# Kernel tuning notes

Measured on AMD Instinct MI355X. Metric: run time of the kernel, lower is better.

The kernel has to match this reference:

```python
import jax, jax.numpy as jnp
import numpy as np

N = 100000
E = 1600000
IN_FEATS = 512
N_HIDDEN = 128
N_CLASSES = 40


def setup_inputs() -> dict:
    key = jax.random.key(0)
    k1, k2, k3, k4, k5, k6, k7 = jax.random.split(key, 7)
    inputs = jax.random.normal(k1, (N, IN_FEATS), dtype=jnp.float32)
    edge_index = jax.random.randint(k2, (2, E), 0, N, dtype=jnp.int64)
    edge_attr = jax.random.uniform(k3, (E,), dtype=jnp.float32)
    # GCNConv params (Glorot-ish scaling)
    W1 = jax.random.normal(k4, (IN_FEATS, N_HIDDEN), dtype=jnp.float32) / np.sqrt(IN_FEATS)
    b1 = jnp.zeros((N_HIDDEN,), dtype=jnp.float32)
    W2 = jax.random.normal(k5, (N_HIDDEN, N_CLASSES), dtype=jnp.float32) / np.sqrt(N_HIDDEN)
    b2 = jnp.zeros((N_CLASSES,), dtype=jnp.float32)
    return {"inputs": inputs, "edge_index": edge_index, "edge_attr": edge_attr,
            "W1": W1, "b1": b1, "W2": W2, "b2": b2}


def gcn_conv(x, W, b, src, dst, edge_weight):
    """GCNConv with normalize=False: linear transform, then edge-weighted
    scatter-sum from src to dst, then bias."""
    m = x @ W                                   # [N, F_out]
    msgs = m[src] * edge_weight[:, None]        # gather + weight, [E, F_out]
    agg = jax.ops.segment_sum(msgs, dst, num_segments=x.shape[0])  # scatter-add
    return agg + b


def reference(inputs, edge_index, edge_attr, W1, b1, W2, b2):
    src, dst = edge_index[0], edge_index[1]
    h = jax.nn.relu(gcn_conv(inputs, W1, b1, src, dst, edge_attr))
    # F.dropout with training=False (eval mode) is identity -> deterministic baseline
    preds = gcn_conv(h, W2, b2, src, dst, edge_attr)
    return jax.nn.log_softmax(preds, axis=1)
```

## Files before the change

### kernel.cpp

```cpp
#include <hip/hip_runtime.h>
#include <hip/hip_bf16.h>
#include <cstdint>

#define N_NODES 100000
#define N_EDGES 1600000
#define F_IN    512
#define F_HID   128
#define F_OUT   40
#define F_OUT_PAD 48

#define BSH    8
#define NB     391
#define BEPT   8
#define BCHUNK 4096
#define GB     391
#define CONVB  140
#define FCAP   6144

typedef short v8s __attribute__((ext_vector_type(8)));
typedef float v4f __attribute__((ext_vector_type(4)));

__device__ __forceinline__ short f2bf(float f) {
    unsigned u = __float_as_uint(f);
    u += 0x7fffu + ((u >> 16) & 1u);
    return (short)(u >> 16);
}

__device__ __forceinline__ float bflo(unsigned u) { return __uint_as_float(u << 16); }
__device__ __forceinline__ float bfhi(unsigned u) { return __uint_as_float(u & 0xffff0000u); }

__device__ __forceinline__ v8s pack8(float4 a, float4 b) {
    v8s r;
    r[0] = f2bf(a.x); r[1] = f2bf(a.y); r[2] = f2bf(a.z); r[3] = f2bf(a.w);
    r[4] = f2bf(b.x); r[5] = f2bf(b.y); r[6] = f2bf(b.z); r[7] = f2bf(b.w);
    return r;
}

__device__ __forceinline__ void gload16(const void* g, void* l) {
    __builtin_amdgcn_global_load_lds(
        (const __attribute__((address_space(1))) void*)g,
        (__attribute__((address_space(3))) void*)l, 16, 0, 0);
}


__global__ __launch_bounds__(512) void k_bhist(const int* __restrict__ dst,
                                               int* __restrict__ bcnt,
                                               const float* __restrict__ W1,
                                               short* __restrict__ WT1,
                                               const float* __restrict__ W2,
                                               short* __restrict__ WT2) {
    if (blockIdx.x >= GB) {
        int i = (blockIdx.x - GB) * 512 + threadIdx.x;
        if (i < F_IN * F_HID) {
            int n = i >> 9, k = i & 511;
            WT1[i] = f2bf(W1[k * F_HID + n]);
        } else {
            int j = i - F_IN * F_HID;
            if (j < F_OUT_PAD * F_HID) {
                int n = j >> 7, k = j & 127;
                WT2[j] = (n < F_OUT) ? f2bf(W2[k * F_OUT + n]) : (short)0;
            }
        }
        return;
    }
    __shared__ int lh[512];
    int tid = threadIdx.x;
    lh[tid] = 0;
    __syncthreads();
    long e0 = (long)blockIdx.x * BCHUNK;
#pragma unroll
    for (int i = 0; i < BEPT; i++) {
        long e = e0 + tid + i * 512;
        if (e < N_EDGES) atomicAdd(&lh[dst[e] >> BSH], 1);
    }
    __syncthreads();
    if (tid < NB && lh[tid]) atomicAdd(&bcnt[tid], lh[tid]);
}

__global__ __launch_bounds__(512) void k_bscan(const int* __restrict__ bcnt,
                                               int* __restrict__ bbase,
                                               int* __restrict__ bcur) {
    __shared__ int sm[512];
    int tid = threadIdx.x;
    int v = (tid < NB) ? bcnt[tid] : 0;
    sm[tid] = v;
    __syncthreads();
    for (int off = 1; off < 512; off <<= 1) {
        int t = (tid >= off) ? sm[tid - off] : 0;
        __syncthreads();
        sm[tid] += t;
        __syncthreads();
    }
    if (tid < NB) {
        int ex = sm[tid] - v;
        bbase[tid] = ex;
        bcur[tid] = ex;
    }
    if (tid == 511) bbase[NB] = sm[511];
}

__global__ __launch_bounds__(512) void k_bscatter(const int* __restrict__ src,
                                                  const int* __restrict__ dst,
                                                  const float* __restrict__ w,
                                                  int* __restrict__ bcur,
                                                  int2* __restrict__ tmp) {
    __shared__ int cntA[512];
    __shared__ int ofsA[512];
    __shared__ int lcur[512];
    __shared__ int gb[512];
    __shared__ __align__(16) int2 recBuf[BCHUNK];
    __shared__ unsigned short bkt[BCHUNK];
    int tid = threadIdx.x;
    long e0 = (long)blockIdx.x * BCHUNK;
    cntA[tid] = 0;
    __syncthreads();

    int dloc[BEPT];
#pragma unroll
    for (int i = 0; i < BEPT; i++) {
        long e = e0 + tid + i * 512;
        int d = (e < N_EDGES) ? dst[e] : -1;
        dloc[i] = d;
        if (d >= 0) atomicAdd(&cntA[d >> BSH], 1);
    }
    __syncthreads();

    int v = cntA[tid];
    ofsA[tid] = v;
    __syncthreads();
    for (int off = 1; off < 512; off <<= 1) {
        int t = (tid >= off) ? ofsA[tid - off] : 0;
        __syncthreads();
        ofsA[tid] += t;
        __syncthreads();
    }
    int excl = ofsA[tid] - v;
    ofsA[tid] = excl;
    lcur[tid] = excl;
    if (tid < NB && v > 0) gb[tid] = atomicAdd(&bcur[tid], v);
    __syncthreads();

#pragma unroll
    for (int i = 0; i < BEPT; i++) {
        int d = dloc[i];
        if (d >= 0) {
            long e = e0 + tid + i * 512;
            int j = d >> BSH;
            int slot = atomicAdd(&lcur[j], 1);
            recBuf[slot] = make_int2(src[e] | ((d & 255) << 17), __float_as_int(w[e]));
            bkt[slot] = (unsigned short)j;
        }
    }
    __syncthreads();

    long rem = N_EDGES - e0;
    int total = (rem < BCHUNK) ? (int)rem : BCHUNK;
    for (int s = tid; s < total; s += 512) {
        int j = bkt[s];
        tmp[gb[j] + (s - ofsA[j])] = recBuf[s];
    }
}

__global__ __launch_bounds__(256) void k_fine(const int2* __restrict__ tmp,
                                              const int* __restrict__ bbase,
                                              int2* __restrict__ rec,
                                              int* __restrict__ rowptr,
                                              int* __restrict__ deg) {
    __shared__ int hist[256];
    __shared__ int ofs[256];
    __shared__ int cur[256];
    __shared__ __align__(16) int2 recOut[FCAP];
    int tid = threadIdx.x, b = blockIdx.x;
    int base = bbase[b];
    int cnt = bbase[b + 1] - base;

    hist[tid] = 0;
    __syncthreads();
    for (int i = tid; i < cnt; i += 256) {
        unsigned u = (unsigned)tmp[base + i].x;
        atomicAdd(&hist[u >> 17], 1);
    }
    __syncthreads();

    int v = hist[tid];
    ofs[tid] = v;
    __syncthreads();
    for (int off = 1; off < 256; off <<= 1) {
        int t = (tid >= off) ? ofs[tid - off] : 0;
        __syncthreads();
        ofs[tid] += t;
        __syncthreads();
    }
    int excl = ofs[tid] - v;
    ofs[tid] = excl;
    cur[tid] = excl;
    int node = (b << BSH) + tid;
    if (node < N_NODES) {
        rowptr[node] = base + excl;
        deg[node] = v;
    }
    __syncthreads();

    if (cnt <= FCAP) {
        for (int i = tid; i < cnt; i += 256) {
            int2 r = tmp[base + i];
            unsigned u = (unsigned)r.x;
            int slot = atomicAdd(&cur[u >> 17], 1);
            recOut[slot] = make_int2((int)(u & 0x1FFFFu), r.y);
        }
        __syncthreads();
        for (int i = tid; i < cnt; i += 256) rec[base + i] = recOut[i];
    } else {
        for (int i = tid; i < cnt; i += 256) {
            int2 r = tmp[base + i];
            unsigned u = (unsigned)r.x;
            int slot = atomicAdd(&cur[u >> 17], 1);
            rec[base + slot] = make_int2((int)(u & 0x1FFFFu), r.y);
        }
    }
}


__global__ __launch_bounds__(256) void k_gemm1(const float* __restrict__ x,
                                               const short* __restrict__ WT1,
                                               unsigned short* __restrict__ m1b) {
    __shared__ __align__(16) float aBuf[2][64 * 32];
    __shared__ __align__(16) short bBuf[2][128 * 32];
    int tid = threadIdx.x, w = tid >> 6, lane = tid & 63;
    int quad = lane >> 4, l16 = lane & 15;
    long rowBase = (long)blockIdx.x * 64;

    int ar = lane >> 3, ac = lane & 7;
    int br = lane >> 2, bc = lane & 3;

    v4f acc[8];
#pragma unroll
    for (int t = 0; t < 8; t++) acc[t] = (v4f){0.f, 0.f, 0.f, 0.f};

    auto stage = [&](int kc, int buf) {
#pragma unroll
        for (int i = 0; i < 2; i++) {
            int rl = w * 16 + i * 8 + ar;
            long rg = rowBase + rl;
            if (rg > N_NODES - 1) rg = N_NODES - 1;
            const float* gp = x + rg * F_IN + kc * 32 + ((ac ^ (rl & 7)) << 2);
            gload16(gp, &aBuf[buf][(w * 16 + i * 8) * 32]);
        }
#pragma unroll
        for (int i = 0; i < 2; i++) {
            int n = w * 32 + i * 16 + br;
            const short* gp = WT1 + n * F_IN + kc * 32 + ((bc ^ ((n >> 1) & 3)) << 3);
            gload16(gp, &bBuf[buf][(w * 32 + i * 16) * 32]);
        }
    };

    stage(0, 0);
#pragma unroll
    for (int kc = 0; kc < 16; kc++) {
        __syncthreads();
        int buf = kc & 1;
        if (kc < 15) stage(kc + 1, buf ^ 1);
        int arow = w * 16 + l16;
        int p0 = (2 * quad) ^ (l16 & 7);
        float4 av0 = *(const float4*)&aBuf[buf][arow * 32 + p0 * 4];
        float4 av1 = *(const float4*)&aBuf[buf][arow * 32 + (p0 ^ 1) * 4];
        v8s af = pack8(av0, av1);
#pragma unroll
        for (int t = 0; t < 8; t++) {
            int n = t * 16 + l16;
            int p = quad ^ ((n >> 1) & 3);
            v8s bf = *(const v8s*)&bBuf[buf][n * 32 + p * 8];
            acc[t] = __builtin_amdgcn_mfma_f32_16x16x32_bf16(af, bf, acc[t], 0, 0, 0);
        }
    }

#pragma unroll
    for (int t = 0; t < 8; t++)
#pragma unroll
        for (int r = 0; r < 4; r++) {
            long row = rowBase + w * 16 + quad * 4 + r;
            if (row < N_NODES)
                m1b[row * F_HID + t * 16 + l16] = (unsigned short)f2bf(acc[t][r]);
        }
}


__global__ void k_agg1(const int2* __restrict__ rec, const int* __restrict__ rowptr,
                       const int* __restrict__ deg, const uint2* __restrict__ m1v,
                       const float* __restrict__ b1, uint2* __restrict__ h2) {
    int node = blockIdx.x * 4 + (threadIdx.x >> 6);
    int lane = threadIdx.x & 63;
    if (node >= N_NODES) return;
    int half = lane >> 5, l32 = lane & 31;
    int start = rowptr[node], cnt = deg[node];

    float a0 = 0.f, a1 = 0.f, a2 = 0.f, a3 = 0.f;
    float c0 = 0.f, c1 = 0.f, c2 = 0.f, c3 = 0.f;

    int nmain = cnt >> 3;
    int ebase = start + half;
    for (int k = 0; k < nmain; k++) {
        int e = ebase + (k << 3);
        int2 r0 = rec[e];
        int2 r1 = rec[e + 2];
        int2 r2 = rec[e + 4];
        int2 r3 = rec[e + 6];
        uint2 g0 = m1v[(long)r0.x * 32 + l32];
        uint2 g1 = m1v[(long)r1.x * 32 + l32];
        uint2 g2 = m1v[(long)r2.x * 32 + l32];
        uint2 g3 = m1v[(long)r3.x * 32 + l32];
        float w0 = __int_as_float(r0.y), w1 = __int_as_float(r1.y);
        float w2 = __int_as_float(r2.y), w3 = __int_as_float(r3.y);
        a0 = fmaf(w0, bflo(g0.x), a0); a1 = fmaf(w0, bfhi(g0.x), a1);
        a2 = fmaf(w0, bflo(g0.y), a2); a3 = fmaf(w0, bfhi(g0.y), a3);
        c0 = fmaf(w1, bflo(g1.x), c0); c1 = fmaf(w1, bfhi(g1.x), c1);
        c2 = fmaf(w1, bflo(g1.y), c2); c3 = fmaf(w1, bfhi(g1.y), c3);
        a0 = fmaf(w2, bflo(g2.x), a0); a1 = fmaf(w2, bfhi(g2.x), a1);
        a2 = fmaf(w2, bflo(g2.y), a2); a3 = fmaf(w2, bfhi(g2.y), a3);
        c0 = fmaf(w3, bflo(g3.x), c0); c1 = fmaf(w3, bfhi(g3.x), c1);
        c2 = fmaf(w3, bflo(g3.y), c2); c3 = fmaf(w3, bfhi(g3.y), c3);
    }
    for (int e = start + (nmain << 3) + half; e < start + cnt; e += 2) {
        int2 r = rec[e];
        uint2 g = m1v[(long)r.x * 32 + l32];
        float w = __int_as_float(r.y);
        a0 = fmaf(w, bflo(g.x), a0); a1 = fmaf(w, bfhi(g.x), a1);
        a2 = fmaf(w, bflo(g.y), a2); a3 = fmaf(w, bfhi(g.y), a3);
    }
    a0 += c0; a1 += c1; a2 += c2; a3 += c3;
    a0 += __shfl_xor(a0, 32);
    a1 += __shfl_xor(a1, 32);
    a2 += __shfl_xor(a2, 32);
    a3 += __shfl_xor(a3, 32);
    if (half == 0) {
        float4 bv = ((const float4*)b1)[l32];
        a0 = fmaxf(a0 + bv.x, 0.f);
        a1 = fmaxf(a1 + bv.y, 0.f);
        a2 = fmaxf(a2 + bv.z, 0.f);
        a3 = fmaxf(a3 + bv.w, 0.f);
        unsigned lo = (unsigned)(unsigned short)f2bf(a0) |
                      ((unsigned)(unsigned short)f2bf(a1) << 16);
        unsigned hi = (unsigned)(unsigned short)f2bf(a2) |
                      ((unsigned)(unsigned short)f2bf(a3) << 16);
        h2[(long)node * 32 + l32] = make_uint2(lo, hi);
    }
}


__global__ __launch_bounds__(256) void k_gemm2(const unsigned short* __restrict__ h,
                                               const short* __restrict__ WT2,
                                               unsigned short* __restrict__ m2b) {
    int wave = threadIdx.x >> 6, lane = threadIdx.x & 63;
    int quad = lane >> 4, l16 = lane & 15;
    long rowBase = ((long)blockIdx.x * 4 + wave) * 16;
    if (rowBase >= N_NODES) return;

    v4f acc[3];
#pragma unroll
    for (int t = 0; t < 3; t++) acc[t] = (v4f){0.f, 0.f, 0.f, 0.f};

    const short* arow = (const short*)h + (rowBase + l16) * (long)F_HID + quad * 8;
    const short* brow = WT2 + l16 * F_HID + quad * 8;
#pragma unroll
    for (int k0 = 0; k0 < F_HID; k0 += 32) {
        v8s af = *reinterpret_cast<const v8s*>(arow + k0);
#pragma unroll
        for (int t = 0; t < 3; t++) {
            v8s bf = *reinterpret_cast<const v8s*>(brow + t * 16 * F_HID + k0);
            acc[t] = __builtin_amdgcn_mfma_f32_16x16x32_bf16(af, bf, acc[t], 0, 0, 0);
        }
    }
#pragma unroll
    for (int r = 0; r < 4; r++) {
        long row = rowBase + quad * 4 + r;
#pragma unroll
        for (int t = 0; t < 3; t++)
            m2b[row * 64 + t * 16 + l16] = (unsigned short)f2bf(acc[t][r]);
        m2b[row * 64 + 48 + l16] = 0;
    }
}


__global__ void k_agg2(const int2* __restrict__ rec, const int* __restrict__ rowptr,
                       const int* __restrict__ deg, const uint2* __restrict__ m2v,
                       const float* __restrict__ b2, float* __restrict__ out) {
    int node = blockIdx.x * 4 + (threadIdx.x >> 6);
    int lane = threadIdx.x & 63;
    if (node >= N_NODES) return;
    int q = lane >> 4, l16 = lane & 15;
    int start = rowptr[node], cnt = deg[node];

    float a0 = 0.f, a1 = 0.f, a2 = 0.f, a3 = 0.f;
    float c0 = 0.f, c1 = 0.f, c2 = 0.f, c3 = 0.f;

    int nmain = cnt >> 3;
    int ebase = start + q;
    for (int k = 0; k < nmain; k++) {
        int e = ebase + (k << 3);
        int2 r0 = rec[e];
        int2 r1 = rec[e + 4];
        uint2 g0 = m2v[(long)r0.x * 16 + l16];
        uint2 g1 = m2v[(long)r1.x * 16 + l16];
        float w0 = __int_as_float(r0.y), w1 = __int_as_float(r1.y);
        a0 = fmaf(w0, bflo(g0.x), a0); a1 = fmaf(w0, bfhi(g0.x), a1);
        a2 = fmaf(w0, bflo(g0.y), a2); a3 = fmaf(w0, bfhi(g0.y), a3);
        c0 = fmaf(w1, bflo(g1.x), c0); c1 = fmaf(w1, bfhi(g1.x), c1);
        c2 = fmaf(w1, bflo(g1.y), c2); c3 = fmaf(w1, bfhi(g1.y), c3);
    }
    for (int e = start + (nmain << 3) + q; e < start + cnt; e += 4) {
        int2 r = rec[e];
        uint2 g = m2v[(long)r.x * 16 + l16];
        float w = __int_as_float(r.y);
        a0 = fmaf(w, bflo(g.x), a0); a1 = fmaf(w, bfhi(g.x), a1);
        a2 = fmaf(w, bflo(g.y), a2); a3 = fmaf(w, bfhi(g.y), a3);
    }
    a0 += c0; a1 += c1; a2 += c2; a3 += c3;
    a0 += __shfl_xor(a0, 16); a0 += __shfl_xor(a0, 32);
    a1 += __shfl_xor(a1, 16); a1 += __shfl_xor(a1, 32);
    a2 += __shfl_xor(a2, 16); a2 += __shfl_xor(a2, 32);
    a3 += __shfl_xor(a3, 16); a3 += __shfl_xor(a3, 32);

    const float NEG = -3.4e38f;
    float v0 = NEG, v1 = NEG, v2 = NEG, v3 = NEG;
    if (l16 < 10) {
        float4 bv = ((const float4*)b2)[l16];
        v0 = a0 + bv.x; v1 = a1 + bv.y; v2 = a2 + bv.z; v3 = a3 + bv.w;
    }
    float m = fmaxf(fmaxf(v0, v1), fmaxf(v2, v3));
#pragma unroll
    for (int off = 1; off < 16; off <<= 1) m = fmaxf(m, __shfl_xor(m, off));
    float s = 0.f;
    if (l16 < 10)
        s = __expf(v0 - m) + __expf(v1 - m) + __expf(v2 - m) + __expf(v3 - m);
#pragma unroll
    for (int off = 1; off < 16; off <<= 1) s += __shfl_xor(s, off);
    if (q == 0 && l16 < 10) {
        float ls = m + __logf(s);
        float4 o;
        o.x = v0 - ls; o.y = v1 - ls; o.z = v2 - ls; o.w = v3 - ls;
        ((float4*)out)[(long)node * 10 + l16] = o;
    }
}


extern "C" void kernel_launch(void* const* d_in, const int* in_sizes, int n_in,
                              void* d_out, int out_size, void* d_ws, size_t ws_size,
                              hipStream_t stream) {
    const float* x  = (const float*)d_in[0];
    const int* ei   = (const int*)d_in[1];
    const int* src  = ei;
    const int* dst  = ei + N_EDGES;
    const float* ew = (const float*)d_in[2];
    const float* W1 = (const float*)d_in[3];
    const float* b1 = (const float*)d_in[4];
    const float* W2 = (const float*)d_in[5];
    const float* b2 = (const float*)d_in[6];
    float* out = (float*)d_out;

    char* ws = (char*)d_ws;
    size_t off = 0;
    auto alloc = [&](size_t bytes) {
        void* p = ws + off;
        off += (bytes + 255) & ~(size_t)255;
        return p;
    };
    unsigned short* m1b  = (unsigned short*)alloc((size_t)N_NODES * F_HID * 2);
    unsigned int*   h    = (unsigned int*)alloc((size_t)N_NODES * F_HID * 2);
    unsigned short* m2b  = (unsigned short*)alloc((size_t)N_NODES * 64 * 2);
    int2*           rec  = (int2*)alloc((size_t)N_EDGES * 8);
    int*          rowptr = (int*)alloc((size_t)N_NODES * 4);
    int*          deg    = (int*)alloc((size_t)N_NODES * 4);
    int*          bCnt   = (int*)alloc(512 * 4);
    int*          bBase  = (int*)alloc(512 * 4);
    int*          bCur   = (int*)alloc(512 * 4);
    short*        WT1    = (short*)alloc((size_t)F_HID * F_IN * 2);
    short*        WT2    = (short*)alloc((size_t)F_OUT_PAD * F_HID * 2);

    int2* tmp = (int2*)m2b;

    hipMemsetAsync(bCnt, 0, 512 * 4, stream);

    k_bhist<<<GB + CONVB, 512, 0, stream>>>(dst, bCnt, W1, WT1, W2, WT2);
    k_bscan<<<1, 512, 0, stream>>>(bCnt, bBase, bCur);
    k_bscatter<<<GB, 512, 0, stream>>>(src, dst, ew, bCur, tmp);
    k_fine<<<NB, 256, 0, stream>>>(tmp, bBase, rec, rowptr, deg);

    k_gemm1<<<(N_NODES + 63) / 64, 256, 0, stream>>>(x, WT1, m1b);
    k_agg1<<<(N_NODES + 3) / 4, 256, 0, stream>>>(rec, rowptr, deg,
                                                  (const uint2*)m1b, b1, (uint2*)h);
    k_gemm2<<<(N_NODES + 63) / 64, 256, 0, stream>>>((const unsigned short*)h, WT2, m2b);
    k_agg2<<<(N_NODES + 3) / 4, 256, 0, stream>>>(rec, rowptr, deg,
                                                  (const uint2*)m2b, b2, out);
}
```

Before: 497.6 us.

## Sort nodes by degree for aggregation and widen gathers to 16-byte loads

Adds a degree histogram in k_fine plus a scan and scatter pass that reorders nodes into degree-sorted buckets (ninfo). Both aggregation kernels then process nodes in that order, so wavefronts that run together see similar degrees and less divergence and load imbalance. The aggregation kernels also switch from 8-byte to 16-byte feature gathers, with more edges handled in parallel per wave and matching shuffle reductions. This costs two extra small kernels, an extra node-info array, and scattered output writes, since the degree order no longer matches node order.

```diff
diff --git a/kernel.cpp b/kernel.cpp
--- a/kernel.cpp
+++ b/kernel.cpp
@@ -16,6 +16,7 @@
 #define GB     391
 #define CONVB  140
 #define FCAP   6144
+#define DBINS  64
 
 typedef short v8s __attribute__((ext_vector_type(8)));
 typedef float v4f __attribute__((ext_vector_type(4)));
@@ -165,16 +166,19 @@
                                               const int* __restrict__ bbase,
                                               int2* __restrict__ rec,
                                               int* __restrict__ rowptr,
-                                              int* __restrict__ deg) {
+                                              int* __restrict__ deg,
+                                              int* __restrict__ dcnt) {
     __shared__ int hist[256];
     __shared__ int ofs[256];
     __shared__ int cur[256];
+    __shared__ int dh[DBINS];
     __shared__ __align__(16) int2 recOut[FCAP];
     int tid = threadIdx.x, b = blockIdx.x;
     int base = bbase[b];
     int cnt = bbase[b + 1] - base;
 
     hist[tid] = 0;
+    if (tid < DBINS) dh[tid] = 0;
     __syncthreads();
     for (int i = tid; i < cnt; i += 256) {
         unsigned u = (unsigned)tmp[base + i].x;
@@ -198,8 +202,10 @@
     if (node < N_NODES) {
         rowptr[node] = base + excl;
         deg[node] = v;
-    }
-    __syncthreads();
+        atomicAdd(&dh[v < DBINS ? v : DBINS - 1], 1);
+    }
+    __syncthreads();
+    if (tid < DBINS && dh[tid]) atomicAdd(&dcnt[tid], dh[tid]);
 
     if (cnt <= FCAP) {
         for (int i = tid; i < cnt; i += 256) {
@@ -218,6 +224,46 @@
             rec[base + slot] = make_int2((int)(u & 0x1FFFFu), r.y);
         }
     }
+}
+
+__global__ __launch_bounds__(DBINS) void k_dscan(const int* __restrict__ dcnt,
+                                                 int* __restrict__ dcur) {
+    __shared__ int sm[DBINS];
+    int tid = threadIdx.x;
+    int v = dcnt[tid];
+    sm[tid] = v;
+    __syncthreads();
+    for (int off = 1; off < DBINS; off <<= 1) {
+        int t = (tid >= off) ? sm[tid - off] : 0;
+        __syncthreads();
+        sm[tid] += t;
+        __syncthreads();
+    }
+    dcur[tid] = sm[tid] - v;
+}
+
+__global__ __launch_bounds__(256) void k_dscatter(const int* __restrict__ rowptr,
+                                                  const int* __restrict__ deg,
+                                                  int* __restrict__ dcur,
+                                                  int4* __restrict__ ninfo) {
+    __shared__ int lh[DBINS];
+    __shared__ int gbase[DBINS];
+    int tid = threadIdx.x;
+    if (tid < DBINS) lh[tid] = 0;
+    __syncthreads();
+    int node = blockIdx.x * 256 + tid;
+    int d = 0, lpos = 0, st = 0, ct = 0;
+    bool valid = node < N_NODES;
+    if (valid) {
+        st = rowptr[node];
+        ct = deg[node];
+        d = ct < DBINS ? ct : DBINS - 1;
+        lpos = atomicAdd(&lh[d], 1);
+    }
+    __syncthreads();
+    if (tid < DBINS && lh[tid]) gbase[tid] = atomicAdd(&dcur[tid], lh[tid]);
+    __syncthreads();
+    if (valid) ninfo[gbase[d] + lpos] = make_int4(node, st, ct, 0);
 }
 
 
@@ -285,64 +331,71 @@
 }
 
 
-__global__ void k_agg1(const int2* __restrict__ rec, const int* __restrict__ rowptr,
-                       const int* __restrict__ deg, const uint2* __restrict__ m1v,
-                       const float* __restrict__ b1, uint2* __restrict__ h2) {
-    int node = blockIdx.x * 4 + (threadIdx.x >> 6);
+__global__ void k_agg1(const int2* __restrict__ rec, const int4* __restrict__ ninfo,
+                       const uint4* __restrict__ m1v, const float* __restrict__ b1,
+                       uint4* __restrict__ h4) {
+    int gid = blockIdx.x * 4 + (threadIdx.x >> 6);
     int lane = threadIdx.x & 63;
-    if (node >= N_NODES) return;
-    int half = lane >> 5, l32 = lane & 31;
-    int start = rowptr[node], cnt = deg[node];
+    if (gid >= N_NODES) return;
+    int4 ni = ninfo[gid];
+    int node = ni.x, start = ni.y, cnt = ni.z;
+    int q = lane >> 4, l16 = lane & 15;
 
     float a0 = 0.f, a1 = 0.f, a2 = 0.f, a3 = 0.f;
+    float a4 = 0.f, a5 = 0.f, a6 = 0.f, a7 = 0.f;
     float c0 = 0.f, c1 = 0.f, c2 = 0.f, c3 = 0.f;
+    float c4 = 0.f, c5 = 0.f, c6 = 0.f, c7 = 0.f;
 
     int nmain = cnt >> 3;
-    int ebase = start + half;
+    int eb = start + q;
     for (int k = 0; k < nmain; k++) {
-        int e = ebase + (k << 3);
+        int e = eb + (k << 3);
         int2 r0 = rec[e];
-        int2 r1 = rec[e + 2];
-        int2 r2 = rec[e + 4];
-        int2 r3 = rec[e + 6];
-        uint2 g0 = m1v[(long)r0.x * 32 + l32];
-        uint2 g1 = m1v[(long)r1.x * 32 + l32];
-        uint2 g2 = m1v[(long)r2.x * 32 + l32];
-        uint2 g3 = m1v[(long)r3.x * 32 + l32];
+        int2 r1 = rec[e + 4];
+        uint4 g0 = m1v[(long)r0.x * 16 + l16];
+        uint4 g1 = m1v[(long)r1.x * 16 + l16];
         float w0 = __int_as_float(r0.y), w1 = __int_as_float(r1.y);
-        float w2 = __int_as_float(r2.y), w3 = __int_as_float(r3.y);
         a0 = fmaf(w0, bflo(g0.x), a0); a1 = fmaf(w0, bfhi(g0.x), a1);
         a2 = fmaf(w0, bflo(g0.y), a2); a3 = fmaf(w0, bfhi(g0.y), a3);
+        a4 = fmaf(w0, bflo(g0.z), a4); a5 = fmaf(w0, bfhi(g0.z), a5);
+        a6 = fmaf(w0, bflo(g0.w), a6); a7 = fmaf(w0, bfhi(g0.w), a7);
         c0 = fmaf(w1, bflo(g1.x), c0); c1 = fmaf(w1, bfhi(g1.x), c1);
         c2 = fmaf(w1, bflo(g1.y), c2); c3 = fmaf(w1, bfhi(g1.y), c3);
-        a0 = fmaf(w2, bflo(g2.x), a0); a1 = fmaf(w2, bfhi(g2.x), a1);
-        a2 = fmaf(w2, bflo(g2.y), a2); a3 = fmaf(w2, bfhi(g2.y), a3);
-        c0 = fmaf(w3, bflo(g3.x), c0); c1 = fmaf(w3, bfhi(g3.x), c1);
-        c2 = fmaf(w3, bflo(g3.y), c2); c3 = fmaf(w3, bfhi(g3.y), c3);
-    }
-    for (int e = start + (nmain << 3) + half; e < start + cnt; e += 2) {
+        c4 = fmaf(w1, bflo(g1.z), c4); c5 = fmaf(w1, bfhi(g1.z), c5);
+        c6 = fmaf(w1, bflo(g1.w), c6); c7 = fmaf(w1, bfhi(g1.w), c7);
+    }
+    for (int e = start + (nmain << 3) + q; e < start + cnt; e += 4) {
         int2 r = rec[e];
-        uint2 g = m1v[(long)r.x * 32 + l32];
+        uint4 g = m1v[(long)r.x * 16 + l16];
         float w = __int_as_float(r.y);
         a0 = fmaf(w, bflo(g.x), a0); a1 = fmaf(w, bfhi(g.x), a1);
         a2 = fmaf(w, bflo(g.y), a2); a3 = fmaf(w, bfhi(g.y), a3);
+        a4 = fmaf(w, bflo(g.z), a4); a5 = fmaf(w, bfhi(g.z), a5);
+        a6 = fmaf(w, bflo(g.w), a6); a7 = fmaf(w, bfhi(g.w), a7);
     }
     a0 += c0; a1 += c1; a2 += c2; a3 += c3;
-    a0 += __shfl_xor(a0, 32);
-    a1 += __shfl_xor(a1, 32);
-    a2 += __shfl_xor(a2, 32);
-    a3 += __shfl_xor(a3, 32);
-    if (half == 0) {
-        float4 bv = ((const float4*)b1)[l32];
-        a0 = fmaxf(a0 + bv.x, 0.f);
-        a1 = fmaxf(a1 + bv.y, 0.f);
-        a2 = fmaxf(a2 + bv.z, 0.f);
-        a3 = fmaxf(a3 + bv.w, 0.f);
-        unsigned lo = (unsigned)(unsigned short)f2bf(a0) |
-                      ((unsigned)(unsigned short)f2bf(a1) << 16);
-        unsigned hi = (unsigned)(unsigned short)f2bf(a2) |
-                      ((unsigned)(unsigned short)f2bf(a3) << 16);
-        h2[(long)node * 32 + l32] = make_uint2(lo, hi);
+    a4 += c4; a5 += c5; a6 += c6; a7 += c7;
+    a0 += __shfl_xor(a0, 16); a0 += __shfl_xor(a0, 32);
+    a1 += __shfl_xor(a1, 16); a1 += __shfl_xor(a1, 32);
+    a2 += __shfl_xor(a2, 16); a2 += __shfl_xor(a2, 32);
+    a3 += __shfl_xor(a3, 16); a3 += __shfl_xor(a3, 32);
+    a4 += __shfl_xor(a4, 16); a4 += __shfl_xor(a4, 32);
+    a5 += __shfl_xor(a5, 16); a5 += __shfl_xor(a5, 32);
+    a6 += __shfl_xor(a6, 16); a6 += __shfl_xor(a6, 32);
+    a7 += __shfl_xor(a7, 16); a7 += __shfl_xor(a7, 32);
+    if (q == 0) {
+        const float4* b4 = (const float4*)b1;
+        float4 bv0 = b4[2 * l16], bv1 = b4[2 * l16 + 1];
+        a0 = fmaxf(a0 + bv0.x, 0.f); a1 = fmaxf(a1 + bv0.y, 0.f);
+        a2 = fmaxf(a2 + bv0.z, 0.f); a3 = fmaxf(a3 + bv0.w, 0.f);
+        a4 = fmaxf(a4 + bv1.x, 0.f); a5 = fmaxf(a5 + bv1.y, 0.f);
+        a6 = fmaxf(a6 + bv1.z, 0.f); a7 = fmaxf(a7 + bv1.w, 0.f);
+        uint4 o;
+        o.x = (unsigned)(unsigned short)f2bf(a0) | ((unsigned)(unsigned short)f2bf(a1) << 16);
+        o.y = (unsigned)(unsigned short)f2bf(a2) | ((unsigned)(unsigned short)f2bf(a3) << 16);
+        o.z = (unsigned)(unsigned short)f2bf(a4) | ((unsigned)(unsigned short)f2bf(a5) << 16);
+        o.w = (unsigned)(unsigned short)f2bf(a6) | ((unsigned)(unsigned short)f2bf(a7) << 16);
+        h4[(long)node * 16 + l16] = o;
     }
 }
 
@@ -381,64 +434,77 @@
 }
 
 
-__global__ void k_agg2(const int2* __restrict__ rec, const int* __restrict__ rowptr,
-                       const int* __restrict__ deg, const uint2* __restrict__ m2v,
-                       const float* __restrict__ b2, float* __restrict__ out) {
-    int node = blockIdx.x * 4 + (threadIdx.x >> 6);
+__global__ void k_agg2(const int2* __restrict__ rec, const int4* __restrict__ ninfo,
+                       const uint4* __restrict__ m2v, const float* __restrict__ b2,
+                       float* __restrict__ out) {
+    int gid = blockIdx.x * 4 + (threadIdx.x >> 6);
     int lane = threadIdx.x & 63;
-    if (node >= N_NODES) return;
-    int q = lane >> 4, l16 = lane & 15;
-    int start = rowptr[node], cnt = deg[node];
+    if (gid >= N_NODES) return;
+    int4 ni = ninfo[gid];
+    int node = ni.x, start = ni.y, cnt = ni.z;
+    int oc = lane >> 3, l8 = lane & 7;
 
     float a0 = 0.f, a1 = 0.f, a2 = 0.f, a3 = 0.f;
-    float c0 = 0.f, c1 = 0.f, c2 = 0.f, c3 = 0.f;
+    float a4 = 0.f, a5 = 0.f, a6 = 0.f, a7 = 0.f;
 
     int nmain = cnt >> 3;
-    int ebase = start + q;
+    int eb = start + oc;
     for (int k = 0; k < nmain; k++) {
-        int e = ebase + (k << 3);
-        int2 r0 = rec[e];
-        int2 r1 = rec[e + 4];
-        uint2 g0 = m2v[(long)r0.x * 16 + l16];
-        uint2 g1 = m2v[(long)r1.x * 16 + l16];
-        float w0 = __int_as_float(r0.y), w1 = __int_as_float(r1.y);
-        a0 = fmaf(w0, bflo(g0.x), a0); a1 = fmaf(w0, bfhi(g0.x), a1);
-        a2 = fmaf(w0, bflo(g0.y), a2); a3 = fmaf(w0, bfhi(g0.y), a3);
-        c0 = fmaf(w1, bflo(g1.x), c0); c1 = fmaf(w1, bfhi(g1.x), c1);
-        c2 = fmaf(w1, bflo(g1.y), c2); c3 = fmaf(w1, bfhi(g1.y), c3);
-    }
-    for (int e = start + (nmain << 3) + q; e < start + cnt; e += 4) {
-        int2 r = rec[e];
-        uint2 g = m2v[(long)r.x * 16 + l16];
+        int2 r = rec[eb + (k << 3)];
+        uint4 g = m2v[(long)r.x * 8 + l8];
         float w = __int_as_float(r.y);
         a0 = fmaf(w, bflo(g.x), a0); a1 = fmaf(w, bfhi(g.x), a1);
         a2 = fmaf(w, bflo(g.y), a2); a3 = fmaf(w, bfhi(g.y), a3);
-    }
-    a0 += c0; a1 += c1; a2 += c2; a3 += c3;
-    a0 += __shfl_xor(a0, 16); a0 += __shfl_xor(a0, 32);
-    a1 += __shfl_xor(a1, 16); a1 += __shfl_xor(a1, 32);
-    a2 += __shfl_xor(a2, 16); a2 += __shfl_xor(a2, 32);
-    a3 += __shfl_xor(a3, 16); a3 += __shfl_xor(a3, 32);
+        a4 = fmaf(w, bflo(g.z), a4); a5 = fmaf(w, bfhi(g.z), a5);
+        a6 = fmaf(w, bflo(g.w), a6); a7 = fmaf(w, bfhi(g.w), a7);
+    }
+    {
+        int e = start + (nmain << 3) + oc;
+        if (e < start + cnt) {
+            int2 r = rec[e];
+            uint4 g = m2v[(long)r.x * 8 + l8];
+            float w = __int_as_float(r.y);
+            a0 = fmaf(w, bflo(g.x), a0); a1 = fmaf(w, bfhi(g.x), a1);
+            a2 = fmaf(w, bflo(g.y), a2); a3 = fmaf(w, bfhi(g.y), a3);
+            a4 = fmaf(w, bflo(g.z), a4); a5 = fmaf(w, bfhi(g.z), a5);
+            a6 = fmaf(w, bflo(g.w), a6); a7 = fmaf(w, bfhi(g.w), a7);
+        }
+    }
+#pragma unroll
+    for (int off = 8; off < 64; off <<= 1) {
+        a0 += __shfl_xor(a0, off); a1 += __shfl_xor(a1, off);
+        a2 += __shfl_xor(a2, off); a3 += __shfl_xor(a3, off);
+        a4 += __shfl_xor(a4, off); a5 += __shfl_xor(a5, off);
+        a6 += __shfl_xor(a6, off); a7 += __shfl_xor(a7, off);
+    }
 
     const float NEG = -3.4e38f;
     float v0 = NEG, v1 = NEG, v2 = NEG, v3 = NEG;
-    if (l16 < 10) {
-        float4 bv = ((const float4*)b2)[l16];
-        v0 = a0 + bv.x; v1 = a1 + bv.y; v2 = a2 + bv.z; v3 = a3 + bv.w;
-    }
-    float m = fmaxf(fmaxf(v0, v1), fmaxf(v2, v3));
-#pragma unroll
-    for (int off = 1; off < 16; off <<= 1) m = fmaxf(m, __shfl_xor(m, off));
+    float v4 = NEG, v5 = NEG, v6 = NEG, v7 = NEG;
+    if (l8 < 5) {
+        const float4* b4 = (const float4*)b2;
+        float4 bv0 = b4[2 * l8], bv1 = b4[2 * l8 + 1];
+        v0 = a0 + bv0.x; v1 = a1 + bv0.y; v2 = a2 + bv0.z; v3 = a3 + bv0.w;
+        v4 = a4 + bv1.x; v5 = a5 + bv1.y; v6 = a6 + bv1.z; v7 = a7 + bv1.w;
+    }
+    float m = fmaxf(fmaxf(fmaxf(v0, v1), fmaxf(v2, v3)),
+                    fmaxf(fmaxf(v4, v5), fmaxf(v6, v7)));
+#pragma unroll
+    for (int off = 1; off < 8; off <<= 1) m = fmaxf(m, __shfl_xor(m, off));
     float s = 0.f;
-    if (l16 < 10)
-        s = __expf(v0 - m) + __expf(v1 - m) + __expf(v2 - m) + __expf(v3 - m);
-#pragma unroll
-    for (int off = 1; off < 16; off <<= 1) s += __shfl_xor(s, off);
-    if (q == 0 && l16 < 10) {
+    if (l8 < 5)
+        s = __expf(v0 - m) + __expf(v1 - m) + __expf(v2 - m) + __expf(v3 - m) +
+            __expf(v4 - m) + __expf(v5 - m) + __expf(v6 - m) + __expf(v7 - m);
+#pragma unroll
+    for (int off = 1; off < 8; off <<= 1) s += __shfl_xor(s, off);
+    if (oc == 0 && l8 < 5) {
         float ls = m + __logf(s);
-        float4 o;
-        o.x = v0 - ls; o.y = v1 - ls; o.z = v2 - ls; o.w = v3 - ls;
-        ((float4*)out)[(long)node * 10 + l16] = o;
+        float4* op = (float4*)(out + (long)node * F_OUT);
+        float4 o0, o1;
+        o0.x = v0 - ls; o0.y = v1 - ls; o0.z = v2 - ls; o0.w = v3 - ls;
+        o1.x = v4 - ls; o1.y = v5 - ls; o1.z = v6 - ls; o1.w = v7 - ls;
+        op[2 * l8] = o0;
+        op[2 * l8 + 1] = o1;
     }
 }
 
@@ -470,25 +536,32 @@
     int2*           rec  = (int2*)alloc((size_t)N_EDGES * 8);
     int*          rowptr = (int*)alloc((size_t)N_NODES * 4);
     int*          deg    = (int*)alloc((size_t)N_NODES * 4);
-    int*          bCnt   = (int*)alloc(512 * 4);
+    int4*         ninfo  = (int4*)alloc((size_t)N_NODES * 16);
+    int*          ctrl   = (int*)alloc(1024 * 4);
     int*          bBase  = (int*)alloc(512 * 4);
     int*          bCur   = (int*)alloc(512 * 4);
     short*        WT1    = (short*)alloc((size_t)F_HID * F_IN * 2);
     short*        WT2    = (short*)alloc((size_t)F_OUT_PAD * F_HID * 2);
 
+    int* bCnt = ctrl;
+    int* dcnt = ctrl + 512;
+    int* dcur = ctrl + 576;
+
     int2* tmp = (int2*)m2b;
 
-    hipMemsetAsync(bCnt, 0, 512 * 4, stream);
+    hipMemsetAsync(ctrl, 0, 576 * 4, stream);
 
     k_bhist<<<GB + CONVB, 512, 0, stream>>>(dst, bCnt, W1, WT1, W2, WT2);
     k_bscan<<<1, 512, 0, stream>>>(bCnt, bBase, bCur);
     k_bscatter<<<GB, 512, 0, stream>>>(src, dst, ew, bCur, tmp);
-    k_fine<<<NB, 256, 0, stream>>>(tmp, bBase, rec, rowptr, deg);
+    k_fine<<<NB, 256, 0, stream>>>(tmp, bBase, rec, rowptr, deg, dcnt);
+    k_dscan<<<1, DBINS, 0, stream>>>(dcnt, dcur);
+    k_dscatter<<<(N_NODES + 255) / 256, 256, 0, stream>>>(rowptr, deg, dcur, ninfo);
 
     k_gemm1<<<(N_NODES + 63) / 64, 256, 0, stream>>>(x, WT1, m1b);
-    k_agg1<<<(N_NODES + 3) / 4, 256, 0, stream>>>(rec, rowptr, deg,
-                                                  (const uint2*)m1b, b1, (uint2*)h);
+    k_agg1<<<(N_NODES + 3) / 4, 256, 0, stream>>>(rec, ninfo, (const uint4*)m1b,
+                                                  b1, (uint4*)h);
     k_gemm2<<<(N_NODES + 63) / 64, 256, 0, stream>>>((const unsigned short*)h, WT2, m2b);
-    k_agg2<<<(N_NODES + 3) / 4, 256, 0, stream>>>(rec, rowptr, deg,
-                                                  (const uint2*)m2b, b2, out);
-}
+    k_agg2<<<(N_NODES + 3) / 4, 256, 0, stream>>>(rec, ninfo, (const uint4*)m2b,
+                                                  b2, out);
+}
```

Measured after the change: 502.9 us. Within noise of the previous version (+1.1%).
